# Performance work log

Hardware: AMD Instinct MI355X
Metric: run time of the kernel (lower is better)

Reference implementation:

```python
import jax, jax.numpy as jnp
import numpy as np

N_NODES = 50000
N_EDGES = 800000
FEAT_DIM = 64
NUM_RELS = 8


def setup_inputs() -> dict:
    key = jax.random.key(0)
    k1, k2, k3, k4, k5 = jax.random.split(key, 5)
    features = jax.random.normal(k1, (N_NODES, FEAT_DIM), dtype=jnp.float32)
    # xavier_uniform with relu gain ~= sqrt(2)*sqrt(6/(D+D))
    limit = np.sqrt(2.0) * np.sqrt(6.0 / (FEAT_DIM + FEAT_DIM))
    weight_r = jax.random.uniform(k2, (NUM_RELS, FEAT_DIM, FEAT_DIM), dtype=jnp.float32,
                                  minval=-limit, maxval=limit)
    src = jax.random.randint(k3, (N_EDGES,), 0, N_NODES, dtype=jnp.int64 if jax.config.jax_enable_x64 else jnp.int32)
    dst = jax.random.randint(k4, (N_EDGES,), 0, N_NODES, dtype=src.dtype)
    etype = jax.random.randint(k5, (N_EDGES,), 0, NUM_RELS, dtype=src.dtype)
    return {"features": features, "weight_r": weight_r, "src": src, "dst": dst, "etype": etype}


def reference(features, weight_r, src, dst, etype):
    N, D = features.shape
    c = 0.2
    # in-degree of each destination node (DGL 'deg' node data)
    deg = jax.ops.segment_sum(jnp.ones(dst.shape, dtype=features.dtype), dst, num_segments=N)
    # relation-batched matmul: h @ W_r for every relation, then gather per edge.
    # [R, N, D] = 8*50000*64 floats -- cheap vs. materializing [E, D, D] weights.
    hw = jnp.einsum('nd,rdf->rnf', features, weight_r)
    msg = hw[etype, src] / deg[dst][:, None]          # [E, D]
    M = jax.ops.segment_sum(msg, dst, num_segments=N)  # scatter-sum mailbox reduce
    updated = jax.nn.relu(c * features + (1.0 - c) * M)
    # DGL only applies reduce to nodes that received messages; others keep h.
    return jnp.where((deg > 0)[:, None], updated, features)
```

## Files before the change

### kernel.cpp

```cpp
#include <hip/hip_runtime.h>
#include <hip/hip_bf16.h>

#define N_NODES 50000
#define N_EDGES 800000
#define FEAT 64
#define NRELS 8
#define NBUCK 196
#define EPB 2048
#define NBP 391
#define BCAP 5120
#define HWB_BLOCKS 782

typedef __attribute__((ext_vector_type(8))) short bf16x8;
typedef __attribute__((ext_vector_type(4))) float f32x4;

static __host__ __device__ inline size_t align256(size_t x) { return (x + 255) & ~(size_t)255; }

__device__ inline unsigned short f2b(float f) {
    unsigned u = __builtin_bit_cast(unsigned, f);
    unsigned r = (u + 0x7fffu + ((u >> 16) & 1u)) >> 16;
    return (unsigned short)r;
}
__device__ inline float b2f(unsigned short u) {
    unsigned v = ((unsigned)u) << 16;
    return __builtin_bit_cast(float, v);
}

__global__ void bfill_kernel(const int* __restrict__ dst, const int* __restrict__ srcv,
                             const int* __restrict__ et, const float* __restrict__ W,
                             int* __restrict__ bcnt, int* __restrict__ tmp,
                             unsigned short* __restrict__ WtT, int E) {
    __shared__ int hist[256];
    __shared__ int base[256];
    __shared__ int lcur[256];
    const int t = threadIdx.x;
    hist[t] = 0; lcur[t] = 0;
    __syncthreads();

    const int4* dst4 = (const int4*)dst;
    const int4* src4 = (const int4*)srcv;
    const int4* et4  = (const int4*)et;
    const int n4 = E >> 2;
    int bk[8], pk[8];
#pragma unroll
    for (int k = 0; k < 2; k++) {
        int i4 = blockIdx.x * 512 + t + k * 256;
        if (i4 < n4) {
            int4 d = dst4[i4];
            int4 s = src4[i4];
            int4 r = et4[i4];
            const int dd[4] = {d.x, d.y, d.z, d.w};
            const int ss[4] = {s.x, s.y, s.z, s.w};
            const int rr[4] = {r.x, r.y, r.z, r.w};
#pragma unroll
            for (int j = 0; j < 4; j++) {
                int idx = k * 4 + j;
                bk[idx] = dd[j] >> 8;
                pk[idx] = (ss[j] & 0xFFFF) | (rr[j] << 16) | ((dd[j] & 255) << 19);
                atomicAdd(&hist[bk[idx]], 1);
            }
        } else {
#pragma unroll
            for (int j = 0; j < 4; j++) bk[k * 4 + j] = -1;
        }
    }
    __syncthreads();
    if (t < NBUCK && hist[t] > 0)
        base[t] = t * BCAP + atomicAdd(&bcnt[t], hist[t]);
    __syncthreads();
#pragma unroll
    for (int k = 0; k < 8; k++) {
        if (bk[k] >= 0) {
            int r = atomicAdd(&lcur[bk[k]], 1);
            int pos = base[bk[k]] + r;
            if (pos < (bk[k] + 1) * BCAP)
                tmp[pos] = pk[k];
        }
    }

    if (blockIdx.x < 32) {
        int i4 = blockIdx.x * 256 + t;
        float4 v = ((const float4*)W)[i4];
        int bse = i4 * 4;
        int f0 = bse & 63;
        int rd = bse >> 6;
        int d  = rd & 63;
        int r  = rd >> 6;
        unsigned short* w0 = WtT + ((size_t)(r * 64 + f0) * 64 + d);
        w0[0 * 64] = f2b(v.x);
        w0[1 * 64] = f2b(v.y);
        w0[2 * 64] = f2b(v.z);
        w0[3 * 64] = f2b(v.w);
    }
}

__global__ void mid_kernel(const int* __restrict__ bcnt, const int* __restrict__ tmp,
                           int* __restrict__ spk, int* __restrict__ off_s,
                           int* __restrict__ off_e,
                           const float* __restrict__ feat,
                           const unsigned short* __restrict__ WtT,
                           unsigned short* __restrict__ hwb, int N) {
    __shared__ unsigned short Fl[64 * 72];
    __shared__ unsigned short Wt[2][64 * 72];
    __shared__ unsigned short Dl[2][64 * 72];
    __shared__ int s[256];
    __shared__ int cur[256];
    const int t = threadIdx.x;

    if (blockIdx.x < NBUCK) {
        const int b = blockIdx.x;
        const int n0 = b * 256;
        const int nn = min(256, N - n0);
        const int s0 = b * BCAP;
        const int s1 = s0 + min(bcnt[b], BCAP);

        s[t] = 0;
        __syncthreads();
        for (int i = s0 + t; i < s1; i += 256)
            atomicAdd(&s[(tmp[i] >> 19) & 255], 1);
        __syncthreads();
        const int myc = s[t];
        for (int o = 1; o < 256; o <<= 1) {
            int u = (t >= o) ? s[t - o] : 0;
            __syncthreads();
            s[t] += u;
            __syncthreads();
        }
        const int ex = s0 + s[t] - myc;
        if (t < nn) {
            off_s[n0 + t] = ex;
            off_e[n0 + t] = ex + myc;
            cur[t] = ex;
        }
        __syncthreads();
        for (int i = s0 + t; i < s1; i += 256) {
            int e = tmp[i];
            int pos = atomicAdd(&cur[(e >> 19) & 255], 1);
            spk[pos] = e;
        }
        return;
    }

    const int n0 = (blockIdx.x - NBUCK) * 64;

    const float4* F4 = (const float4*)feat;
#pragma unroll
    for (int i = 0; i < 4; i++) {
        int idx = t + 256 * i;
        int n = idx >> 4;
        int c = idx & 15;
        int gn = n0 + n;
        float4 v = make_float4(0.f, 0.f, 0.f, 0.f);
        if (gn < N) v = F4[(size_t)gn * 16 + c];
        ushort4 b;
        b.x = f2b(v.x); b.y = f2b(v.y); b.z = f2b(v.z); b.w = f2b(v.w);
        *(ushort4*)&Fl[n * 72 + c * 4] = b;
    }
    {
        const bf16x8* wsrc = (const bf16x8*)WtT;
#pragma unroll
        for (int j = 0; j < 2; j++) {
            int idx = t + 256 * j;
            int f = idx >> 3, d0 = (idx & 7) * 8;
            *(bf16x8*)&Wt[0][f * 72 + d0] = wsrc[idx];
        }
    }
    __syncthreads();

    const int w    = t >> 6;
    const int l    = t & 63;
    const int col  = l & 15;
    const int quad = l >> 4;

    const int arow = (w * 16 + col) * 72 + quad * 8;
    bf16x8 a0 = *(const bf16x8*)&Fl[arow];
    bf16x8 a1 = *(const bf16x8*)&Fl[arow + 32];

    for (int r = 0; r < NRELS; r++) {
        bf16x8 w0, w1;
        if (r + 1 < NRELS) {
            const bf16x8* wsrc = (const bf16x8*)(WtT + (size_t)(r + 1) * 4096);
            w0 = wsrc[t];
            w1 = wsrc[t + 256];
        }

        const unsigned short* wbuf = Wt[r & 1];
        unsigned short* dbuf = Dl[r & 1];
#pragma unroll
        for (int ft = 0; ft < 4; ft++) {
            const int brow = (ft * 16 + col) * 72 + quad * 8;
            bf16x8 b0 = *(const bf16x8*)&wbuf[brow];
            bf16x8 b1 = *(const bf16x8*)&wbuf[brow + 32];
            f32x4 acc = {0.f, 0.f, 0.f, 0.f};
            acc = __builtin_amdgcn_mfma_f32_16x16x32_bf16(a0, b0, acc, 0, 0, 0);
            acc = __builtin_amdgcn_mfma_f32_16x16x32_bf16(a1, b1, acc, 0, 0, 0);
#pragma unroll
            for (int i = 0; i < 4; i++)
                dbuf[(w * 16 + quad * 4 + i) * 72 + ft * 16 + col] = f2b(acc[i]);
        }
        if (r + 1 < NRELS) {
            int f0 = t >> 3, d0 = (t & 7) * 8;
            *(bf16x8*)&Wt[(r + 1) & 1][f0 * 72 + d0] = w0;
            int idx = t + 256;
            int f1 = idx >> 3, d1 = (idx & 7) * 8;
            *(bf16x8*)&Wt[(r + 1) & 1][f1 * 72 + d1] = w1;
        }
        __syncthreads();

        unsigned short* dstp = hwb + ((size_t)r * N + n0) * 64;
#pragma unroll
        for (int j0 = 0; j0 < 2; j0++) {
            int j = t + 256 * j0;
            int row = j >> 3, c = j & 7;
            if (n0 + row < N) {
                bf16x8 dv = *(const bf16x8*)&dbuf[row * 72 + c * 8];
                *(bf16x8*)(dstp + row * 64 + c * 8) = dv;
            }
        }
    }
}

__global__ void reduce_kernel(const int* __restrict__ off_s, const int* __restrict__ off_e,
                              const int* __restrict__ spk,
                              const unsigned short* __restrict__ hwb,
                              const float* __restrict__ feat,
                              float* __restrict__ out, int N) {
    const int node = blockIdx.x * 4 + (threadIdx.x >> 6);
    if (node >= N) return;
    const int lane = threadIdx.x & 63;
    const int g = lane >> 3, q = lane & 7;

    const int b = off_s[node], e = off_e[node];
    const int deg = e - b;

    float acc[8] = {0.f, 0.f, 0.f, 0.f, 0.f, 0.f, 0.f, 0.f};
    for (int i = b + g; i < e; i += 32) {
        int pk0 = spk[i];
        int pk1 = (i + 8  < e) ? spk[i + 8]  : -1;
        int pk2 = (i + 16 < e) ? spk[i + 16] : -1;
        int pk3 = (i + 24 < e) ? spk[i + 24] : -1;
        int s0 = pk0 & 0xFFFF, r0 = (pk0 >> 16) & 7;
        bf16x8 u0 = *(const bf16x8*)(hwb + ((size_t)r0 * N + s0) * 64 + q * 8);
        if (pk1 >= 0) {
            int s1 = pk1 & 0xFFFF, r1 = (pk1 >> 16) & 7;
            bf16x8 u1 = *(const bf16x8*)(hwb + ((size_t)r1 * N + s1) * 64 + q * 8);
            if (pk2 >= 0) {
                int s2 = pk2 & 0xFFFF, r2 = (pk2 >> 16) & 7;
                bf16x8 u2 = *(const bf16x8*)(hwb + ((size_t)r2 * N + s2) * 64 + q * 8);
                if (pk3 >= 0) {
                    int s3 = pk3 & 0xFFFF, r3 = (pk3 >> 16) & 7;
                    bf16x8 u3 = *(const bf16x8*)(hwb + ((size_t)r3 * N + s3) * 64 + q * 8);
#pragma unroll
                    for (int k = 0; k < 8; k++)
                        acc[k] += (b2f((unsigned short)u0[k]) + b2f((unsigned short)u1[k]))
                                + (b2f((unsigned short)u2[k]) + b2f((unsigned short)u3[k]));
                } else {
#pragma unroll
                    for (int k = 0; k < 8; k++)
                        acc[k] += b2f((unsigned short)u0[k]) + b2f((unsigned short)u1[k])
                                + b2f((unsigned short)u2[k]);
                }
            } else {
#pragma unroll
                for (int k = 0; k < 8; k++)
                    acc[k] += b2f((unsigned short)u0[k]) + b2f((unsigned short)u1[k]);
            }
        } else {
#pragma unroll
            for (int k = 0; k < 8; k++) acc[k] += b2f((unsigned short)u0[k]);
        }
    }
#pragma unroll
    for (int k = 0; k < 8; k++) {
        acc[k] += __shfl_xor(acc[k], 8);
        acc[k] += __shfl_xor(acc[k], 16);
        acc[k] += __shfl_xor(acc[k], 32);
    }

    if (g == 0) {
        const float4* fp = (const float4*)feat + (size_t)node * 16 + q * 2;
        float4 f0 = fp[0], f1 = fp[1];
        float4 r0, r1;
        if (deg > 0) {
            float inv = 0.8f / (float)deg;
            r0.x = fmaxf(0.2f * f0.x + acc[0] * inv, 0.f);
            r0.y = fmaxf(0.2f * f0.y + acc[1] * inv, 0.f);
            r0.z = fmaxf(0.2f * f0.z + acc[2] * inv, 0.f);
            r0.w = fmaxf(0.2f * f0.w + acc[3] * inv, 0.f);
            r1.x = fmaxf(0.2f * f1.x + acc[4] * inv, 0.f);
            r1.y = fmaxf(0.2f * f1.y + acc[5] * inv, 0.f);
            r1.z = fmaxf(0.2f * f1.z + acc[6] * inv, 0.f);
            r1.w = fmaxf(0.2f * f1.w + acc[7] * inv, 0.f);
        } else {
            r0 = f0; r1 = f1;
        }
        float4* op = (float4*)out + (size_t)node * 16 + q * 2;
        op[0] = r0;
        op[1] = r1;
    }
}

__global__ void degf_kernel(const int* __restrict__ dst, float* __restrict__ deg, int E) {
    int e = blockIdx.x * blockDim.x + threadIdx.x;
    if (e < E) atomicAdd(deg + dst[e], 1.0f);
}

__global__ void otf_kernel(const int* __restrict__ src, const int* __restrict__ dst,
                           const int* __restrict__ et, const float* __restrict__ feat,
                           const float* __restrict__ W, float* __restrict__ out, int E) {
    int wid = (blockIdx.x * blockDim.x + threadIdx.x) >> 6;
    int l = threadIdx.x & 63;
    if (wid >= E) return;
    int s = src[wid], dd = dst[wid], r = et[wid];
    float fv = feat[(size_t)s * 64 + l];
    const float* Wr = W + (size_t)r * 4096;
    float acc = 0.f;
#pragma unroll
    for (int d = 0; d < 64; d++) {
        float a = __shfl(fv, d);
        acc += a * Wr[d * 64 + l];
    }
    atomicAdd(out + (size_t)dd * 64 + l, acc);
}

__global__ void final_kernel(const float* __restrict__ feat, const float* __restrict__ deg,
                             float* __restrict__ out, int N) {
    int i = blockIdx.x * blockDim.x + threadIdx.x;
    if (i >= N * 16) return;
    int n = i >> 4;
    float d = deg[n];
    float4 f = ((const float4*)feat)[i];
    float4 m = ((float4*)out)[i];
    float4 res;
    if (d > 0.f) {
        float inv = 0.8f / d;
        res.x = fmaxf(0.2f * f.x + m.x * inv, 0.f);
        res.y = fmaxf(0.2f * f.y + m.y * inv, 0.f);
        res.z = fmaxf(0.2f * f.z + m.z * inv, 0.f);
        res.w = fmaxf(0.2f * f.w + m.w * inv, 0.f);
    } else {
        res = f;
    }
    ((float4*)out)[i] = res;
}

extern "C" void kernel_launch(void* const* d_in, const int* in_sizes, int n_in,
                              void* d_out, int out_size, void* d_ws, size_t ws_size,
                              hipStream_t stream) {
    const float* feat = (const float*)d_in[0];
    const float* W    = (const float*)d_in[1];
    const int*   src  = (const int*)d_in[2];
    const int*   dst  = (const int*)d_in[3];
    const int*   et   = (const int*)d_in[4];
    float* out = (float*)d_out;

    const int N = N_NODES, E = N_EDGES;

    char* p = (char*)d_ws;
    int* bcnt  = (int*)p;  p += align256((size_t)NBUCK * 4);
    int* off_s = (int*)p;  p += align256((size_t)N * 4);
    int* off_e = (int*)p;  p += align256((size_t)N * 4);
    int* tmp   = (int*)p;  p += align256((size_t)NBUCK * BCAP * 4);
    int* spk   = (int*)p;  p += align256((size_t)NBUCK * BCAP * 4);
    unsigned short* WtT = (unsigned short*)p;
    p += align256((size_t)NRELS * FEAT * FEAT * 2);
    unsigned short* hwb = (unsigned short*)p;
    p += (size_t)NRELS * N * FEAT * 2;
    size_t need_full = (size_t)(p - (char*)d_ws);

    if (ws_size >= need_full) {
        hipMemsetAsync(bcnt, 0, (size_t)NBUCK * 4, stream);
        bfill_kernel<<<NBP, 256, 0, stream>>>(dst, src, et, W, bcnt, tmp, WtT, E);
        mid_kernel<<<NBUCK + HWB_BLOCKS, 256, 0, stream>>>(bcnt, tmp, spk, off_s, off_e,
                                                           feat, WtT, hwb, N);
        reduce_kernel<<<(N + 3) / 4, 256, 0, stream>>>(off_s, off_e, spk, hwb, feat, out, N);
    } else {
        float* deg = (float*)d_ws;
        hipMemsetAsync(out, 0, (size_t)N * FEAT * 4, stream);
        hipMemsetAsync(deg, 0, (size_t)N * 4, stream);
        degf_kernel<<<(E + 255) / 256, 256, 0, stream>>>(dst, deg, E);
        otf_kernel<<<(E + 3) / 4, 256, 0, stream>>>(src, dst, et, feat, W, out, E);
        final_kernel<<<(N * 16 + 255) / 256, 256, 0, stream>>>(feat, deg, out, N);
    }
}
```

Before: 127.7 us.

## Aggregate raw features per relation, then apply relation weights after reduction

Instead of precomputing h@W_r for all 8 relations over every node and gathering those per edge, the new path converts features to bf16 once and gathers raw source features. These are summed per destination node into per-relation LDS buckets, then multiplied by the eight weight matrices with MFMA before the epilogue. This removes writing and gathering the large 8xNxD bf16 intermediate and fuses reduce with the transform. In exchange, each edge is handled serially by one 8-lane group doing read-modify-write into LDS, the per-relation sums are rounded to bf16 before the matmul, and the kernel needs 64 KB of LDS per block, which limits occupancy.

```diff
diff --git a/kernel.cpp b/kernel.cpp
--- a/kernel.cpp
+++ b/kernel.cpp
@@ -9,7 +9,9 @@
 #define EPB 2048
 #define NBP 391
 #define BCAP 5120
-#define HWB_BLOCKS 782
+#define FB_BLOCKS 782
+#define NPB 32
+#define FUSE_BLOCKS 1563
 
 typedef __attribute__((ext_vector_type(8))) short bf16x8;
 typedef __attribute__((ext_vector_type(4))) float f32x4;
@@ -98,11 +100,7 @@
                            int* __restrict__ spk, int* __restrict__ off_s,
                            int* __restrict__ off_e,
                            const float* __restrict__ feat,
-                           const unsigned short* __restrict__ WtT,
-                           unsigned short* __restrict__ hwb, int N) {
-    __shared__ unsigned short Fl[64 * 72];
-    __shared__ unsigned short Wt[2][64 * 72];
-    __shared__ unsigned short Dl[2][64 * 72];
+                           unsigned short* __restrict__ Fb, int N) {
     __shared__ int s[256];
     __shared__ int cur[256];
     const int t = threadIdx.x;
@@ -141,162 +139,167 @@
         return;
     }
 
-    const int n0 = (blockIdx.x - NBUCK) * 64;
-
-    const float4* F4 = (const float4*)feat;
+    const int fbb = blockIdx.x - NBUCK;
+    const int node = fbb * 64 + (t >> 2);
+    if (node >= N) return;
+    const int seg = t & 3;
+    const float4* F4 = (const float4*)feat + (size_t)node * 16 + seg * 4;
+    float4 v0 = F4[0], v1 = F4[1], v2 = F4[2], v3 = F4[3];
+    bf16x8 b0, b1;
+    b0[0] = (short)f2b(v0.x); b0[1] = (short)f2b(v0.y);
+    b0[2] = (short)f2b(v0.z); b0[3] = (short)f2b(v0.w);
+    b0[4] = (short)f2b(v1.x); b0[5] = (short)f2b(v1.y);
+    b0[6] = (short)f2b(v1.z); b0[7] = (short)f2b(v1.w);
+    b1[0] = (short)f2b(v2.x); b1[1] = (short)f2b(v2.y);
+    b1[2] = (short)f2b(v2.z); b1[3] = (short)f2b(v2.w);
+    b1[4] = (short)f2b(v3.x); b1[5] = (short)f2b(v3.y);
+    b1[6] = (short)f2b(v3.z); b1[7] = (short)f2b(v3.w);
+    *(bf16x8*)(Fb + (size_t)node * 64 + seg * 16)     = b0;
+    *(bf16x8*)(Fb + (size_t)node * 64 + seg * 16 + 8) = b1;
+}
+
+__global__ __launch_bounds__(256, 2) void fuse_kernel(
+    const int* __restrict__ off_s, const int* __restrict__ off_e,
+    const int* __restrict__ spk, const unsigned short* __restrict__ Fb,
+    const unsigned short* __restrict__ WtT, const float* __restrict__ feat,
+    float* __restrict__ out, int N) {
+    __shared__ float SL[NRELS * NPB * 64];
+    const int t = threadIdx.x;
+    const int n0 = blockIdx.x * NPB;
+    const int nn = min(NPB, N - n0);
+    const int w = t >> 6, l = t & 63, col = l & 15, quad = l >> 4;
+
+    bf16x8 bw0[NRELS], bw1[NRELS];
+#pragma unroll
+    for (int r = 0; r < NRELS; r++) {
+        const unsigned short* wp = WtT + (size_t)r * 4096 + ((w * 16 + col) * 64 + quad * 8);
+        bw0[r] = *(const bf16x8*)wp;
+        bw1[r] = *(const bf16x8*)(wp + 32);
+    }
+
+    {
+        f32x4 z = {0.f, 0.f, 0.f, 0.f};
+#pragma unroll
+        for (int i = 0; i < 16; i++)
+            *(f32x4*)&SL[(i * 256 + t) * 4] = z;
+    }
+    __syncthreads();
+
+    const int gid = t >> 3, q = t & 7;
+    if (gid < nn) {
+        const int gn = n0 + gid;
+        const int rowbase = gid * 64 + 8 * (q ^ (gid & 7));
+        const int b = off_s[gn], e = off_e[gn];
+        if (b < e) {
+            int pk = spk[b];
+            bf16x8 u = *(const bf16x8*)(Fb + (size_t)(pk & 0xFFFF) * 64 + q * 8);
+            for (int i = b; i < e; i++) {
+                int pk_n = 0;
+                bf16x8 u_n = u;
+                if (i + 1 < e) {
+                    pk_n = spk[i + 1];
+                    u_n = *(const bf16x8*)(Fb + (size_t)(pk_n & 0xFFFF) * 64 + q * 8);
+                }
+                const int r = (pk >> 16) & 7;
+                float* p = &SL[r * (NPB * 64) + rowbase];
+                float4 x0 = *(float4*)p;
+                float4 x1 = *(float4*)(p + 4);
+                x0.x += b2f((unsigned short)u[0]);
+                x0.y += b2f((unsigned short)u[1]);
+                x0.z += b2f((unsigned short)u[2]);
+                x0.w += b2f((unsigned short)u[3]);
+                x1.x += b2f((unsigned short)u[4]);
+                x1.y += b2f((unsigned short)u[5]);
+                x1.z += b2f((unsigned short)u[6]);
+                x1.w += b2f((unsigned short)u[7]);
+                *(float4*)p = x0;
+                *(float4*)(p + 4) = x1;
+                pk = pk_n; u = u_n;
+            }
+        }
+    }
+    __syncthreads();
+
+    f32x4 acc0 = {0.f, 0.f, 0.f, 0.f}, acc1 = {0.f, 0.f, 0.f, 0.f};
+    const int o0 = 8 * (quad ^ (col & 7));
+    const int o1 = 8 * ((quad + 4) ^ (col & 7));
+#pragma unroll
+    for (int r = 0; r < NRELS; r++) {
+        const float* Sr = &SL[r * (NPB * 64)];
+        {
+            const float* ap = Sr + col * 64;
+            float4 fa = *(const float4*)(ap + o0);
+            float4 fb = *(const float4*)(ap + o0 + 4);
+            float4 fc = *(const float4*)(ap + o1);
+            float4 fd = *(const float4*)(ap + o1 + 4);
+            bf16x8 a0, a1;
+            a0[0] = (short)f2b(fa.x); a0[1] = (short)f2b(fa.y);
+            a0[2] = (short)f2b(fa.z); a0[3] = (short)f2b(fa.w);
+            a0[4] = (short)f2b(fb.x); a0[5] = (short)f2b(fb.y);
+            a0[6] = (short)f2b(fb.z); a0[7] = (short)f2b(fb.w);
+            a1[0] = (short)f2b(fc.x); a1[1] = (short)f2b(fc.y);
+            a1[2] = (short)f2b(fc.z); a1[3] = (short)f2b(fc.w);
+            a1[4] = (short)f2b(fd.x); a1[5] = (short)f2b(fd.y);
+            a1[6] = (short)f2b(fd.z); a1[7] = (short)f2b(fd.w);
+            acc0 = __builtin_amdgcn_mfma_f32_16x16x32_bf16(a0, bw0[r], acc0, 0, 0, 0);
+            acc0 = __builtin_amdgcn_mfma_f32_16x16x32_bf16(a1, bw1[r], acc0, 0, 0, 0);
+        }
+        {
+            const float* ap = Sr + (16 + col) * 64;
+            float4 fa = *(const float4*)(ap + o0);
+            float4 fb = *(const float4*)(ap + o0 + 4);
+            float4 fc = *(const float4*)(ap + o1);
+            float4 fd = *(const float4*)(ap + o1 + 4);
+            bf16x8 a0, a1;
+            a0[0] = (short)f2b(fa.x); a0[1] = (short)f2b(fa.y);
+            a0[2] = (short)f2b(fa.z); a0[3] = (short)f2b(fa.w);
+            a0[4] = (short)f2b(fb.x); a0[5] = (short)f2b(fb.y);
+            a0[6] = (short)f2b(fb.z); a0[7] = (short)f2b(fb.w);
+            a1[0] = (short)f2b(fc.x); a1[1] = (short)f2b(fc.y);
+            a1[2] = (short)f2b(fc.z); a1[3] = (short)f2b(fc.w);
+            a1[4] = (short)f2b(fd.x); a1[5] = (short)f2b(fd.y);
+            a1[6] = (short)f2b(fd.z); a1[7] = (short)f2b(fd.w);
+            acc1 = __builtin_amdgcn_mfma_f32_16x16x32_bf16(a0, bw0[r], acc1, 0, 0, 0);
+            acc1 = __builtin_amdgcn_mfma_f32_16x16x32_bf16(a1, bw1[r], acc1, 0, 0, 0);
+        }
+    }
+    __syncthreads();
+
 #pragma unroll
     for (int i = 0; i < 4; i++) {
-        int idx = t + 256 * i;
-        int n = idx >> 4;
-        int c = idx & 15;
-        int gn = n0 + n;
-        float4 v = make_float4(0.f, 0.f, 0.f, 0.f);
-        if (gn < N) v = F4[(size_t)gn * 16 + c];
-        ushort4 b;
-        b.x = f2b(v.x); b.y = f2b(v.y); b.z = f2b(v.z); b.w = f2b(v.w);
-        *(ushort4*)&Fl[n * 72 + c * 4] = b;
-    }
+        SL[(quad * 4 + i) * 64 + w * 16 + col]        = acc0[i];
+        SL[(16 + quad * 4 + i) * 64 + w * 16 + col]   = acc1[i];
+    }
+    __syncthreads();
+
     {
-        const bf16x8* wsrc = (const bf16x8*)WtT;
-#pragma unroll
-        for (int j = 0; j < 2; j++) {
-            int idx = t + 256 * j;
-            int f = idx >> 3, d0 = (idx & 7) * 8;
-            *(bf16x8*)&Wt[0][f * 72 + d0] = wsrc[idx];
-        }
-    }
-    __syncthreads();
-
-    const int w    = t >> 6;
-    const int l    = t & 63;
-    const int col  = l & 15;
-    const int quad = l >> 4;
-
-    const int arow = (w * 16 + col) * 72 + quad * 8;
-    bf16x8 a0 = *(const bf16x8*)&Fl[arow];
-    bf16x8 a1 = *(const bf16x8*)&Fl[arow + 32];
-
-    for (int r = 0; r < NRELS; r++) {
-        bf16x8 w0, w1;
-        if (r + 1 < NRELS) {
-            const bf16x8* wsrc = (const bf16x8*)(WtT + (size_t)(r + 1) * 4096);
-            w0 = wsrc[t];
-            w1 = wsrc[t + 256];
-        }
-
-        const unsigned short* wbuf = Wt[r & 1];
-        unsigned short* dbuf = Dl[r & 1];
-#pragma unroll
-        for (int ft = 0; ft < 4; ft++) {
-            const int brow = (ft * 16 + col) * 72 + quad * 8;
-            bf16x8 b0 = *(const bf16x8*)&wbuf[brow];
-            bf16x8 b1 = *(const bf16x8*)&wbuf[brow + 32];
-            f32x4 acc = {0.f, 0.f, 0.f, 0.f};
-            acc = __builtin_amdgcn_mfma_f32_16x16x32_bf16(a0, b0, acc, 0, 0, 0);
-            acc = __builtin_amdgcn_mfma_f32_16x16x32_bf16(a1, b1, acc, 0, 0, 0);
-#pragma unroll
-            for (int i = 0; i < 4; i++)
-                dbuf[(w * 16 + quad * 4 + i) * 72 + ft * 16 + col] = f2b(acc[i]);
-        }
-        if (r + 1 < NRELS) {
-            int f0 = t >> 3, d0 = (t & 7) * 8;
-            *(bf16x8*)&Wt[(r + 1) & 1][f0 * 72 + d0] = w0;
-            int idx = t + 256;
-            int f1 = idx >> 3, d1 = (idx & 7) * 8;
-            *(bf16x8*)&Wt[(r + 1) & 1][f1 * 72 + d1] = w1;
-        }
-        __syncthreads();
-
-        unsigned short* dstp = hwb + ((size_t)r * N + n0) * 64;
-#pragma unroll
-        for (int j0 = 0; j0 < 2; j0++) {
-            int j = t + 256 * j0;
-            int row = j >> 3, c = j & 7;
-            if (n0 + row < N) {
-                bf16x8 dv = *(const bf16x8*)&dbuf[row * 72 + c * 8];
-                *(bf16x8*)(dstp + row * 64 + c * 8) = dv;
+        const int n = t >> 3;
+        if (n < nn) {
+            const int gn = n0 + n;
+            const int f0 = (t & 7) * 8;
+            const int deg = off_e[gn] - off_s[gn];
+            float4 m0 = *(const float4*)&SL[n * 64 + f0];
+            float4 m1 = *(const float4*)&SL[n * 64 + f0 + 4];
+            const float4* fp = (const float4*)feat + (size_t)gn * 16 + (f0 >> 2);
+            float4 h0 = fp[0], h1 = fp[1];
+            float4 r0, r1;
+            if (deg > 0) {
+                float inv = 0.8f / (float)deg;
+                r0.x = fmaxf(0.2f * h0.x + m0.x * inv, 0.f);
+                r0.y = fmaxf(0.2f * h0.y + m0.y * inv, 0.f);
+                r0.z = fmaxf(0.2f * h0.z + m0.z * inv, 0.f);
+                r0.w = fmaxf(0.2f * h0.w + m0.w * inv, 0.f);
+                r1.x = fmaxf(0.2f * h1.x + m1.x * inv, 0.f);
+                r1.y = fmaxf(0.2f * h1.y + m1.y * inv, 0.f);
+                r1.z = fmaxf(0.2f * h1.z + m1.z * inv, 0.f);
+                r1.w = fmaxf(0.2f * h1.w + m1.w * inv, 0.f);
+            } else {
+                r0 = h0; r1 = h1;
             }
-        }
-    }
-}
-
-__global__ void reduce_kernel(const int* __restrict__ off_s, const int* __restrict__ off_e,
-                              const int* __restrict__ spk,
-                              const unsigned short* __restrict__ hwb,
-                              const float* __restrict__ feat,
-                              float* __restrict__ out, int N) {
-    const int node = blockIdx.x * 4 + (threadIdx.x >> 6);
-    if (node >= N) return;
-    const int lane = threadIdx.x & 63;
-    const int g = lane >> 3, q = lane & 7;
-
-    const int b = off_s[node], e = off_e[node];
-    const int deg = e - b;
-
-    float acc[8] = {0.f, 0.f, 0.f, 0.f, 0.f, 0.f, 0.f, 0.f};
-    for (int i = b + g; i < e; i += 32) {
-        int pk0 = spk[i];
-        int pk1 = (i + 8  < e) ? spk[i + 8]  : -1;
-        int pk2 = (i + 16 < e) ? spk[i + 16] : -1;
-        int pk3 = (i + 24 < e) ? spk[i + 24] : -1;
-        int s0 = pk0 & 0xFFFF, r0 = (pk0 >> 16) & 7;
-        bf16x8 u0 = *(const bf16x8*)(hwb + ((size_t)r0 * N + s0) * 64 + q * 8);
-        if (pk1 >= 0) {
-            int s1 = pk1 & 0xFFFF, r1 = (pk1 >> 16) & 7;
-            bf16x8 u1 = *(const bf16x8*)(hwb + ((size_t)r1 * N + s1) * 64 + q * 8);
-            if (pk2 >= 0) {
-                int s2 = pk2 & 0xFFFF, r2 = (pk2 >> 16) & 7;
-                bf16x8 u2 = *(const bf16x8*)(hwb + ((size_t)r2 * N + s2) * 64 + q * 8);
-                if (pk3 >= 0) {
-                    int s3 = pk3 & 0xFFFF, r3 = (pk3 >> 16) & 7;
-                    bf16x8 u3 = *(const bf16x8*)(hwb + ((size_t)r3 * N + s3) * 64 + q * 8);
-#pragma unroll
-                    for (int k = 0; k < 8; k++)
-                        acc[k] += (b2f((unsigned short)u0[k]) + b2f((unsigned short)u1[k]))
-                                + (b2f((unsigned short)u2[k]) + b2f((unsigned short)u3[k]));
-                } else {
-#pragma unroll
-                    for (int k = 0; k < 8; k++)
-                        acc[k] += b2f((unsigned short)u0[k]) + b2f((unsigned short)u1[k])
-                                + b2f((unsigned short)u2[k]);
-                }
-            } else {
-#pragma unroll
-                for (int k = 0; k < 8; k++)
-                    acc[k] += b2f((unsigned short)u0[k]) + b2f((unsigned short)u1[k]);
-            }
-        } else {
-#pragma unroll
-            for (int k = 0; k < 8; k++) acc[k] += b2f((unsigned short)u0[k]);
-        }
-    }
-#pragma unroll
-    for (int k = 0; k < 8; k++) {
-        acc[k] += __shfl_xor(acc[k], 8);
-        acc[k] += __shfl_xor(acc[k], 16);
-        acc[k] += __shfl_xor(acc[k], 32);
-    }
-
-    if (g == 0) {
-        const float4* fp = (const float4*)feat + (size_t)node * 16 + q * 2;
-        float4 f0 = fp[0], f1 = fp[1];
-        float4 r0, r1;
-        if (deg > 0) {
-            float inv = 0.8f / (float)deg;
-            r0.x = fmaxf(0.2f * f0.x + acc[0] * inv, 0.f);
-            r0.y = fmaxf(0.2f * f0.y + acc[1] * inv, 0.f);
-            r0.z = fmaxf(0.2f * f0.z + acc[2] * inv, 0.f);
-            r0.w = fmaxf(0.2f * f0.w + acc[3] * inv, 0.f);
-            r1.x = fmaxf(0.2f * f1.x + acc[4] * inv, 0.f);
-            r1.y = fmaxf(0.2f * f1.y + acc[5] * inv, 0.f);
-            r1.z = fmaxf(0.2f * f1.z + acc[6] * inv, 0.f);
-            r1.w = fmaxf(0.2f * f1.w + acc[7] * inv, 0.f);
-        } else {
-            r0 = f0; r1 = f1;
-        }
-        float4* op = (float4*)out + (size_t)node * 16 + q * 2;
-        op[0] = r0;
-        op[1] = r1;
+            float4* op = (float4*)out + (size_t)gn * 16 + (f0 >> 2);
+            op[0] = r0;
+            op[1] = r1;
+        }
     }
 }
 
@@ -364,16 +367,17 @@
     int* spk   = (int*)p;  p += align256((size_t)NBUCK * BCAP * 4);
     unsigned short* WtT = (unsigned short*)p;
     p += align256((size_t)NRELS * FEAT * FEAT * 2);
-    unsigned short* hwb = (unsigned short*)p;
-    p += (size_t)NRELS * N * FEAT * 2;
+    unsigned short* Fb = (unsigned short*)p;
+    p += align256((size_t)N * FEAT * 2);
     size_t need_full = (size_t)(p - (char*)d_ws);
 
     if (ws_size >= need_full) {
         hipMemsetAsync(bcnt, 0, (size_t)NBUCK * 4, stream);
         bfill_kernel<<<NBP, 256, 0, stream>>>(dst, src, et, W, bcnt, tmp, WtT, E);
-        mid_kernel<<<NBUCK + HWB_BLOCKS, 256, 0, stream>>>(bcnt, tmp, spk, off_s, off_e,
-                                                           feat, WtT, hwb, N);
-        reduce_kernel<<<(N + 3) / 4, 256, 0, stream>>>(off_s, off_e, spk, hwb, feat, out, N);
+        mid_kernel<<<NBUCK + FB_BLOCKS, 256, 0, stream>>>(bcnt, tmp, spk, off_s, off_e,
+                                                          feat, Fb, N);
+        fuse_kernel<<<FUSE_BLOCKS, 256, 0, stream>>>(off_s, off_e, spk, Fb, WtT,
+                                                     feat, out, N);
     } else {
         float* deg = (float*)d_ws;
         hipMemsetAsync(out, 0, (size_t)N * FEAT * 4, stream);
```

Result: slower. 180.5 us (+41.3%).
